# Performance work log

Hardware: AMD Instinct MI355X
Metric: run time of the kernel (lower is better)

Reference implementation:

```python
import jax, jax.numpy as jnp
import numpy as np

# --- dims (match init_kwargs / input_specs) ---
B = 2048          # batch
ALEN = 32         # action history length
TP = 16           # prediction horizon
STATE_DIM = 17
ACTION_DIM = 6
TERMS = 33        # s_recon_terms (Fourier ILT terms)
HID = 64          # hidden_units
GRU_H = 32        # hidden_units // 2
OUT = STATE_DIM   # output_dim
LAT = STATE_DIM + 2  # laplace latent dim (state + 2-d action latent)
# Fourier ILT (Dubner-Abate) constants, as in torchlaplace Fourier defaults
ALPHA = 1e-3
TOL = 1e-2        # 10 * alpha
SCALE = 2.0
PI = np.pi


def _gru_layer(x, Wih, Whh, bih, bhh):
    """PyTorch-semantics GRU layer. x: (B, L, D) -> all hidden states (B, L, H)."""
    nb, H = x.shape[0], Whh.shape[1]
    xw = x @ Wih.T + bih  # (B, L, 3H), precomputed input projections

    def step(h, xw_t):
        gh = h @ Whh.T + bhh
        xr, xz, xn = jnp.split(xw_t, 3, axis=-1)
        hr, hz, hn = jnp.split(gh, 3, axis=-1)
        r = jax.nn.sigmoid(xr + hr)
        z = jax.nn.sigmoid(xz + hz)
        n = jnp.tanh(xn + r * hn)
        h = (1.0 - z) * n + z * h
        return h, h

    h0 = jnp.zeros((nb, H), x.dtype)
    _, outs = jax.lax.scan(step, h0, jnp.swapaxes(xw, 0, 1))
    return jnp.swapaxes(outs, 0, 1)


def setup_inputs() -> dict:
    key = jax.random.key(0)
    ks = jax.random.split(key, 20)
    w = lambda k, shape, s=0.1: jax.random.normal(k, shape, jnp.float32) * s
    d = {}
    d["in_batch_obs"] = jax.random.normal(ks[0], (B, STATE_DIM), jnp.float32)
    d["in_batch_action"] = jax.random.normal(ks[1], (B, ALEN, ACTION_DIM), jnp.float32)
    # positive query times (offset avoids t ~ 0 on the Bromwich contour)
    d["ts_pred"] = jax.random.uniform(ks[2], (B, TP), jnp.float32) + 0.1
    # GRU layer 0
    d["gru_Wih0"] = w(ks[3], (3 * GRU_H, ACTION_DIM))
    d["gru_Whh0"] = w(ks[4], (3 * GRU_H, GRU_H))
    d["gru_bih0"] = jnp.zeros((3 * GRU_H,), jnp.float32)
    d["gru_bhh0"] = jnp.zeros((3 * GRU_H,), jnp.float32)
    # GRU layer 1
    d["gru_Wih1"] = w(ks[5], (3 * GRU_H, GRU_H))
    d["gru_Whh1"] = w(ks[6], (3 * GRU_H, GRU_H))
    d["gru_bih1"] = jnp.zeros((3 * GRU_H,), jnp.float32)
    d["gru_bhh1"] = jnp.zeros((3 * GRU_H,), jnp.float32)
    # encoder linear out -> 2-d action latent
    d["enc_Wout"] = w(ks[7], (2, GRU_H))
    d["enc_bout"] = jnp.zeros((2,), jnp.float32)
    # Laplace representation MLP
    d["mlp_W1"] = w(ks[8], (HID, 2 * TERMS + LAT))
    d["mlp_b1"] = jnp.zeros((HID,), jnp.float32)
    d["mlp_W2"] = w(ks[9], (HID, HID))
    d["mlp_b2"] = jnp.zeros((HID,), jnp.float32)
    d["mlp_W3"] = w(ks[10], (2 * OUT * TERMS, HID))
    d["mlp_b3"] = jnp.zeros((2 * OUT * TERMS,), jnp.float32)
    return d


def reference(in_batch_obs, in_batch_action, ts_pred,
              gru_Wih0, gru_Whh0, gru_bih0, gru_bhh0,
              gru_Wih1, gru_Whh1, gru_bih1, gru_bhh1,
              enc_Wout, enc_bout,
              mlp_W1, mlp_b1, mlp_W2, mlp_b2, mlp_W3, mlp_b3):
    # normalize=False branch
    batch_obs = in_batch_obs
    batch_action = in_batch_action / 3.0

    # ---- ReverseGRUEncoder: flip time, 2-layer GRU, last output -> latent(2) ----
    x = batch_action[:, ::-1, :]
    h1 = _gru_layer(x, gru_Wih0, gru_Whh0, gru_bih0, gru_bhh0)
    h2 = _gru_layer(h1, gru_Wih1, gru_Whh1, gru_bih1, gru_bhh1)
    p_action = h2[:, -1, :] @ enc_Wout.T + enc_bout        # (B, 2)
    p = jnp.concatenate([batch_obs, p_action], axis=1)     # (B, LAT)

    # ---- Fourier ILT contour query points s_k = gamma + i*pi*k/T ----
    t = ts_pred                                            # (B, TP)
    Tc = SCALE * t
    gamma = ALPHA - np.log(TOL) / Tc                       # (B, TP)
    k = jnp.arange(TERMS, dtype=t.dtype)                   # (TERMS,)
    s_im = PI * k / Tc[..., None]                          # (B, TP, TERMS)
    s_re = jnp.broadcast_to(gamma[..., None], s_im.shape)
    # Riemann-sphere coordinates of s
    sq = s_re * s_re + s_im * s_im
    theta_s = jnp.arctan2(s_im, s_re)
    phi_s = jnp.arcsin((sq - 1.0) / (sq + 1.0))

    # ---- LaplaceRepresentationFunc (MLP) per (batch, time) point ----
    pt = jnp.broadcast_to(p[:, None, :], (p.shape[0], t.shape[1], LAT))
    inp = jnp.concatenate([theta_s, phi_s, pt], axis=-1)   # (B, TP, 2*TERMS+LAT)
    h = jnp.tanh(inp @ mlp_W1.T + mlp_b1)
    h = jnp.tanh(h @ mlp_W2.T + mlp_b2)
    out = (h @ mlp_W3.T + mlp_b3).reshape(p.shape[0], t.shape[1], 2 * OUT, TERMS)
    theta = jnp.tanh(out[..., :OUT, :]) * PI               # (B, TP, OUT, TERMS)
    phi = jnp.tanh(out[..., OUT:, :]) * (PI / 2.0)         # phi_scale=pi -> (-pi/2, pi/2)

    # ---- inverse stereographic projection: sphere -> complex F(s) ----
    denom = 1.0 - jnp.sin(phi)
    cphi = jnp.cos(phi)
    Fr = jnp.cos(theta) * cphi / denom
    Fi = jnp.sin(theta) * cphi / denom                     # (B, TP, OUT, TERMS)

    # ---- Fourier-series line integral (k=0 term halved), real arithmetic ----
    ang = PI * k * (t / Tc)[..., None]                     # (B, TP, TERMS)
    wk = jnp.where(k == 0, 0.5, 1.0)
    series = wk * (Fr * jnp.cos(ang)[:, :, None, :] - Fi * jnp.sin(ang)[:, :, None, :])
    f = (jnp.exp(gamma * t) / Tc)[..., None] * series.sum(axis=-1)  # (B, TP, OUT)
    return jnp.squeeze(f)


if __name__ == "__main__":
    outs = reference(**setup_inputs())
    print(outs.shape)
```

## Files before the change

### kernel.cpp

```cpp
#include <hip/hip_runtime.h>
#include <math.h>

#define PI_F 3.14159265358979323846f
#define PI_2F 1.57079632679489662f

typedef __attribute__((ext_vector_type(8))) short short8;
typedef __attribute__((ext_vector_type(4))) float f32x4;
#define MFMA16(A,B,C) __builtin_amdgcn_mfma_f32_16x16x32_bf16(A,B,C,0,0,0)
#define SCHED_FENCE() __builtin_amdgcn_sched_barrier(0)

__device__ __forceinline__ float sigm_f(float x) {
    return __fdividef(1.0f, 1.0f + __expf(-x));
}
__device__ __forceinline__ float tanh_f(float x) {
    float xc = fminf(fmaxf(x, -9.0f), 9.0f);
    float e = __expf(2.0f * xc);
    return 1.0f - __fdividef(2.0f, e + 1.0f);
}
__device__ __forceinline__ float atan01(float z) {
    float z2 = z * z;
    float p = fmaf(z2, -0.0117212f, 0.05265332f);
    p = fmaf(z2, p, -0.11643287f);
    p = fmaf(z2, p, 0.19354346f);
    p = fmaf(z2, p, -0.33262347f);
    p = fmaf(z2, p, 0.99997726f);
    return z * p;
}
__device__ __forceinline__ float atan_pos(float x) {
    bool big = x > 1.0f;
    float z = big ? __fdividef(1.0f, x) : x;
    float p = atan01(z);
    return big ? (PI_2F - p) : p;
}
__device__ __forceinline__ unsigned short f2bf(float x) {
    unsigned int u = __float_as_uint(x);
    return (unsigned short)((u + 0x7FFFu + ((u >> 16) & 1u)) >> 16);
}
__device__ __forceinline__ float bf2f(unsigned short h) {
    return __uint_as_float(((unsigned int)h) << 16);
}
__device__ __forceinline__ float lo16f(unsigned int u) { return __uint_as_float(u << 16); }
__device__ __forceinline__ float hi16f(unsigned int u) { return __uint_as_float(u & 0xFFFF0000u); }

__device__ __forceinline__ float lap_term(float at, float ap, int k) {
    float th = tanh_f(at) * PI_F;
    float ph = tanh_f(ap) * (0.5f * PI_F);
    float sph = __sinf(ph), cph = __cosf(ph);
    float rdv = __fdividef(1.0f, 1.0f - sph);
    float tr = __sinf((k & 1) ? th : th + PI_2F);
    float w = (k == 0) ? 0.5f : 1.0f;
    w = ((k + 1) & 2) ? -w : w;
    return w * tr * cph * rdv;
}

__global__ __launch_bounds__(256)
void w3pack_kernel(const float* __restrict__ W3, unsigned short* __restrict__ pk)
{
    int i = blockIdx.x * 256 + threadIdx.x;
    if (i >= 34 * 4096) return;
    int u    = i >> 12;
    int rem  = i & 4095;
    int r    = rem >> 8;
    int rem2 = rem & 255;
    int pl   = rem2 >> 6;
    int s    = rem2 & 63;
    int o = u >> 1, mt = u & 1;
    int row = o * 33 + mt * 16 + r + ((pl >= 2) ? 561 : 0);
    float x = W3[row * 64 + s];
    unsigned short h = f2bf(x);
    pk[i] = (pl & 1) ? f2bf(x - bf2f(h)) : h;
}

__global__ __launch_bounds__(128)
void gru_kernel(const float* __restrict__ act,
                const float* __restrict__ Wih0, const float* __restrict__ Whh0,
                const float* __restrict__ bih0, const float* __restrict__ bhh0,
                const float* __restrict__ Wih1, const float* __restrict__ Whh1,
                const float* __restrict__ bih1, const float* __restrict__ bhh1,
                const float* __restrict__ encW, const float* __restrict__ encb,
                float* __restrict__ p_out)
{
    __shared__ __align__(16) float wih0_l[6 * 128];
    __shared__ __align__(16) unsigned short whh0_p[16 * 32 * 8];
    __shared__ __align__(16) unsigned short wih1_p[16 * 32 * 8];
    __shared__ __align__(16) unsigned short whh1_p[16 * 32 * 8];
    __shared__ float enc_l[64];
    __shared__ __align__(16) float xbuf[4 * 32 * 6];
    __shared__ __align__(16) float hbuf0[4][32];
    __shared__ __align__(16) float hbuf1[4][32];

    const int tid = threadIdx.x;

    for (int idx = tid; idx < 96 * 6; idx += 128) {
        int r = idx / 6, c = idx - r * 6;
        wih0_l[c * 128 + (r & 31) * 4 + (r >> 5)] = Wih0[idx];
    }
    for (int idx = tid; idx < 96 * 32; idx += 128) {
        int r = idx >> 5, c = idx & 31;
        int g = r >> 5, j = r & 31;
        int d = ((c >> 1) * 32 + j) * 8 + g * 2 + (c & 1);
        whh0_p[d] = f2bf(Whh0[idx]);
        wih1_p[d] = f2bf(Wih1[idx]);
        whh1_p[d] = f2bf(Whh1[idx]);
    }
    if (tid < 64) {
        int o = tid >> 5, j = tid & 31;
        enc_l[j * 2 + o] = encW[o * 32 + j];
    }
    {
        const float inv3 = (1.0f / 3.0f);
        int base = blockIdx.x * (4 * 32 * 6);
        for (int idx = tid; idx < 4 * 32 * 6; idx += 128)
            xbuf[idx] = act[base + idx] * inv3;
    }
    __syncthreads();

    const int s = tid >> 5;
    const int j = tid & 31;
    const int b = blockIdx.x * 4 + s;
    const int j4 = j * 4;

    const float bi0r = bih0[j], bi0z = bih0[32 + j], bi0n = bih0[64 + j];
    const float bh0r = bhh0[j], bh0z = bhh0[32 + j], bh0n = bhh0[64 + j];
    const float bi1r = bih1[j], bi1z = bih1[32 + j], bi1n = bih1[64 + j];
    const float bh1r = bhh1[j], bh1z = bhh1[32 + j], bh1n = bhh1[64 + j];

    float* hb0 = &hbuf0[s][0];
    float* hb1 = &hbuf1[s][0];
    hb0[j] = 0.0f;
    hb1[j] = 0.0f;
    float h0 = 0.0f, h1 = 0.0f;
    const float* xs = &xbuf[s * 192];

    for (int t = 0; t < 32; ++t) {
        const float* xt = &xs[(31 - t) * 6];

        float ar = bi0r, az = bi0z, an = bi0n;
        #pragma unroll
        for (int d = 0; d < 6; ++d) {
            float xv = xt[d];
            const float4 w = *reinterpret_cast<const float4*>(&wih0_l[d * 128 + j4]);
            ar = fmaf(xv, w.x, ar); az = fmaf(xv, w.y, az); an = fmaf(xv, w.z, an);
        }
        {
            float gr0 = bh0r, gz0 = bh0z, gn0 = bh0n;
            float gr1 = 0.0f, gz1 = 0.0f, gn1 = 0.0f;
            #pragma unroll
            for (int ib = 0; ib < 32; ib += 4) {
                const float4 h4 = *reinterpret_cast<const float4*>(&hb0[ib]);
                const uint4 wA = *reinterpret_cast<const uint4*>(&whh0_p[((ib >> 1) * 32 + j) * 8]);
                const uint4 wB = *reinterpret_cast<const uint4*>(&whh0_p[((ib >> 1) * 32 + j + 32) * 8]);
                gr0 = fmaf(h4.x, lo16f(wA.x), gr0); gr1 = fmaf(h4.y, hi16f(wA.x), gr1);
                gz0 = fmaf(h4.x, lo16f(wA.y), gz0); gz1 = fmaf(h4.y, hi16f(wA.y), gz1);
                gn0 = fmaf(h4.x, lo16f(wA.z), gn0); gn1 = fmaf(h4.y, hi16f(wA.z), gn1);
                gr0 = fmaf(h4.z, lo16f(wB.x), gr0); gr1 = fmaf(h4.w, hi16f(wB.x), gr1);
                gz0 = fmaf(h4.z, lo16f(wB.y), gz0); gz1 = fmaf(h4.w, hi16f(wB.y), gz1);
                gn0 = fmaf(h4.z, lo16f(wB.z), gn0); gn1 = fmaf(h4.w, hi16f(wB.z), gn1);
            }
            float r = sigm_f(ar + gr0 + gr1);
            float z = sigm_f(az + gz0 + gz1);
            float n = tanh_f(an + r * (gn0 + gn1));
            h0 = (1.0f - z) * n + z * h0;
            hb0[j] = h0;
        }
        {
            float a1r0 = bi1r, a1z0 = bi1z, a1n0 = bi1n;
            float a1r1 = 0.0f, a1z1 = 0.0f, a1n1 = 0.0f;
            float g1r0 = bh1r, g1z0 = bh1z, g1n0 = bh1n;
            float g1r1 = 0.0f, g1z1 = 0.0f, g1n1 = 0.0f;
            #pragma unroll
            for (int ib = 0; ib < 32; ib += 4) {
                const float4 ha = *reinterpret_cast<const float4*>(&hb0[ib]);
                const float4 hg = *reinterpret_cast<const float4*>(&hb1[ib]);
                const uint4 aA = *reinterpret_cast<const uint4*>(&wih1_p[((ib >> 1) * 32 + j) * 8]);
                const uint4 aB = *reinterpret_cast<const uint4*>(&wih1_p[((ib >> 1) * 32 + j + 32) * 8]);
                const uint4 gA = *reinterpret_cast<const uint4*>(&whh1_p[((ib >> 1) * 32 + j) * 8]);
                const uint4 gB = *reinterpret_cast<const uint4*>(&whh1_p[((ib >> 1) * 32 + j + 32) * 8]);
                a1r0 = fmaf(ha.x, lo16f(aA.x), a1r0); a1r1 = fmaf(ha.y, hi16f(aA.x), a1r1);
                a1z0 = fmaf(ha.x, lo16f(aA.y), a1z0); a1z1 = fmaf(ha.y, hi16f(aA.y), a1z1);
                a1n0 = fmaf(ha.x, lo16f(aA.z), a1n0); a1n1 = fmaf(ha.y, hi16f(aA.z), a1n1);
                a1r0 = fmaf(ha.z, lo16f(aB.x), a1r0); a1r1 = fmaf(ha.w, hi16f(aB.x), a1r1);
                a1z0 = fmaf(ha.z, lo16f(aB.y), a1z0); a1z1 = fmaf(ha.w, hi16f(aB.y), a1z1);
                a1n0 = fmaf(ha.z, lo16f(aB.z), a1n0); a1n1 = fmaf(ha.w, hi16f(aB.z), a1n1);
                g1r0 = fmaf(hg.x, lo16f(gA.x), g1r0); g1r1 = fmaf(hg.y, hi16f(gA.x), g1r1);
                g1z0 = fmaf(hg.x, lo16f(gA.y), g1z0); g1z1 = fmaf(hg.y, hi16f(gA.y), g1z1);
                g1n0 = fmaf(hg.x, lo16f(gA.z), g1n0); g1n1 = fmaf(hg.y, hi16f(gA.z), g1n1);
                g1r0 = fmaf(hg.z, lo16f(gB.x), g1r0); g1r1 = fmaf(hg.w, hi16f(gB.x), g1r1);
                g1z0 = fmaf(hg.z, lo16f(gB.y), g1z0); g1z1 = fmaf(hg.w, hi16f(gB.y), g1z1);
                g1n0 = fmaf(hg.z, lo16f(gB.z), g1n0); g1n1 = fmaf(hg.w, hi16f(gB.z), g1n1);
            }
            float r1 = sigm_f(a1r0 + a1r1 + g1r0 + g1r1);
            float z1 = sigm_f(a1z0 + a1z1 + g1z0 + g1z1);
            float n1 = tanh_f(a1n0 + a1n1 + r1 * (g1n0 + g1n1));
            h1 = (1.0f - z1) * n1 + z1 * h1;
            hb1[j] = h1;
        }
    }

    float v0 = h1 * enc_l[j * 2 + 0];
    float v1 = h1 * enc_l[j * 2 + 1];
    #pragma unroll
    for (int off = 16; off > 0; off >>= 1) {
        v0 += __shfl_xor(v0, off, 32);
        v1 += __shfl_xor(v1, off, 32);
    }
    if (j == 0) {
        p_out[b * 2 + 0] = v0 + encb[0];
        p_out[b * 2 + 1] = v1 + encb[1];
    }
}


__device__ __forceinline__ void load_B(const unsigned short* b_hi, const unsigned short* b_lo,
                                       int itm, int ksl,
                                       short8& Bh0, short8& Bh1, short8& Bl0, short8& Bl1)
{
    const int sw = (itm & 7) << 3;
    const int kx0 = ksl ^ sw;
    const int kx1 = (32 + ksl) ^ sw;
    Bh0 = *reinterpret_cast<const short8*>(&b_hi[itm * 64 + kx0]);
    Bh1 = *reinterpret_cast<const short8*>(&b_hi[itm * 64 + kx1]);
    Bl0 = *reinterpret_cast<const short8*>(&b_lo[itm * 64 + kx0]);
    Bl1 = *reinterpret_cast<const short8*>(&b_lo[itm * 64 + kx1]);
}

__device__ __forceinline__ float lap4(f32x4 aT, f32x4 aP, const float* __restrict__ b3,
                                      int rd, int kbase)
{
    float s = 0.0f;
    #pragma unroll
    for (int r = 0; r < 4; ++r)
        s += lap_term(aT[r] + b3[rd + r], aP[r] + b3[rd + r + 561], kbase + r);
    return s;
}

__device__ __forceinline__ float k32_term(const float* __restrict__ W3f,
                                          const float* __restrict__ b3,
                                          const float* __restrict__ h2f,
                                          int o, int l4)
{
    const int rt = o * 33 + 32;
    const float* wtr = W3f + rt * 64;
    const float* wpr = W3f + (rt + 561) * 64;
    float at = b3[rt], ap = b3[rt + 561];
    #pragma unroll
    for (int c = 0; c < 16; ++c) {
        const float4 g4 = *reinterpret_cast<const float4*>(&h2f[c * 256 + l4]);
        at = fmaf(g4.x, wtr[c * 4 + 0], at);
        at = fmaf(g4.y, wtr[c * 4 + 1], at);
        at = fmaf(g4.z, wtr[c * 4 + 2], at);
        at = fmaf(g4.w, wtr[c * 4 + 3], at);
        ap = fmaf(g4.x, wpr[c * 4 + 0], ap);
        ap = fmaf(g4.y, wpr[c * 4 + 1], ap);
        ap = fmaf(g4.z, wpr[c * 4 + 2], ap);
        ap = fmaf(g4.w, wpr[c * 4 + 3], ap);
    }
    return lap_term(at, ap, 32);
}

#define UNIT_G(G, EACC) { \
    short8 Bh0, Bh1, Bl0, Bl1; \
    load_B(b_hi, b_lo, (G) * 16 + lm, ksl, Bh0, Bh1, Bl0, Bl1); \
    f32x4 accT = {0.0f, 0.0f, 0.0f, 0.0f}; \
    { \
        const short8 A0 = *reinterpret_cast<const short8*>(au + 0); \
        const short8 A1 = *reinterpret_cast<const short8*>(au + 64); \
        const short8 A2 = *reinterpret_cast<const short8*>(au + 128); \
        const short8 A3 = *reinterpret_cast<const short8*>(au + 192); \
        accT = MFMA16(A0, Bh0, accT); accT = MFMA16(A1, Bh1, accT); \
        accT = MFMA16(A0, Bl0, accT); accT = MFMA16(A1, Bl1, accT); \
        accT = MFMA16(A2, Bh0, accT); accT = MFMA16(A3, Bh1, accT); \
    } \
    f32x4 accP = {0.0f, 0.0f, 0.0f, 0.0f}; \
    { \
        const short8 A0 = *reinterpret_cast<const short8*>(au + 256); \
        const short8 A1 = *reinterpret_cast<const short8*>(au + 320); \
        const short8 A2 = *reinterpret_cast<const short8*>(au + 384); \
        const short8 A3 = *reinterpret_cast<const short8*>(au + 448); \
        accP = MFMA16(A0, Bh0, accP); accP = MFMA16(A1, Bh1, accP); \
        accP = MFMA16(A0, Bl0, accP); accP = MFMA16(A1, Bl1, accP); \
        accP = MFMA16(A2, Bh0, accP); accP = MFMA16(A3, Bh1, accP); \
    } \
    EACC += lap4(accT, accP, b3, rd, kbase); \
    SCHED_FENCE(); \
}

__global__ __launch_bounds__(512, 4)
void mlp_kernel(const float* __restrict__ obs, const float* __restrict__ ts,
                const float* __restrict__ p_act,
                const float* __restrict__ W1, const float* __restrict__ b1,
                const float* __restrict__ W2, const float* __restrict__ b2,
                const unsigned short* __restrict__ w3pk,
                const float* __restrict__ b3,
                const float* __restrict__ W3f,
                float* __restrict__ out)
{
    __shared__ __align__(16) float h1t[16 * 256];
    __shared__ __align__(16) unsigned short b_hi[64 * 64];
    __shared__ __align__(16) unsigned short b_lo[64 * 64];
    __shared__ __align__(16) float vtp_lds[33 * 128];
    __shared__ float f_lds[17 * 64];
    __shared__ float f16k32[64];
    __shared__ float scale_lds[64];

    float* h2f = vtp_lds;

    const int tid = threadIdx.x;
    const int wq = __builtin_amdgcn_readfirstlane(tid >> 6);
    const int l = tid & 63;
    const int l4 = l * 4;
    const int item = blockIdx.x * 64 + l;
    const int b = item >> 4;
    const int obase = wq * 8;

    const float t = ts[item];
    const float rTc = __fdividef(0.5f, t);
    const float gamma = 0.001f + 4.6051701859880913680f * rTc;

    if (wq == 0) scale_lds[l] = __expf(gamma * t) * rTc;

    const float gam2 = gamma * gamma;
    const float rg = __fdividef(1.0f, gamma);
    const float pirTc = PI_F * rTc;

    for (int k = wq; k < 33; k += 8) {
        float sim = (float)k * pirTc;
        float vth = atan_pos(sim * rg);
        float sq = fmaf(sim, sim, gam2);
        float vph = fmaf(-2.0f, atan01(rsqrtf(sq)), PI_2F);
        vtp_lds[k * 128 + (l << 1) + 0] = vth;
        vtp_lds[k * 128 + (l << 1) + 1] = vph;
    }
    __syncthreads();

    {
        float acc[8];
        #pragma unroll
        for (int oo = 0; oo < 8; ++oo) acc[oo] = b1[obase + oo];
        const float* w1b = W1 + obase * 85;

        for (int k = 0; k < 33; ++k) {
            const float2 tp = *reinterpret_cast<const float2*>(&vtp_lds[k * 128 + (l << 1)]);
            #pragma unroll
            for (int oo = 0; oo < 8; ++oo) {
                acc[oo] = fmaf(tp.x, w1b[oo * 85 + k], acc[oo]);
                acc[oo] = fmaf(tp.y, w1b[oo * 85 + 33 + k], acc[oo]);
            }
        }
        #pragma unroll
        for (int j = 0; j < 19; ++j) {
            float pv = (j < 17) ? obs[b * 17 + j] : p_act[b * 2 + (j - 17)];
            #pragma unroll
            for (int oo = 0; oo < 8; ++oo)
                acc[oo] = fmaf(pv, w1b[oo * 85 + 66 + j], acc[oo]);
        }
        #pragma unroll
        for (int oo = 0; oo < 8; ++oo) {
            int o = obase + oo;
            h1t[(o >> 2) * 256 + l4 + (o & 3)] = tanh_f(acc[oo]);
        }
    }
    __syncthreads();

    {
        float acc[8];
        #pragma unroll
        for (int oo = 0; oo < 8; ++oo) acc[oo] = b2[obase + oo];
        #pragma unroll
        for (int c = 0; c < 16; ++c) {
            const float4 g4 = *reinterpret_cast<const float4*>(&h1t[c * 256 + l4]);
            #pragma unroll
            for (int oo = 0; oo < 8; ++oo) {
                const float* wr = W2 + (obase + oo) * 64 + c * 4;
                acc[oo] = fmaf(g4.x, wr[0], acc[oo]);
                acc[oo] = fmaf(g4.y, wr[1], acc[oo]);
                acc[oo] = fmaf(g4.z, wr[2], acc[oo]);
                acc[oo] = fmaf(g4.w, wr[3], acc[oo]);
            }
        }
        const int sw = (l & 7) << 3;
        #pragma unroll
        for (int p = 0; p < 4; ++p) {
            float v0 = tanh_f(acc[2 * p + 0]);
            float v1 = tanh_f(acc[2 * p + 1]);
            int o0 = obase + 2 * p;
            h2f[((o0 + 0) >> 2) * 256 + l4 + ((o0 + 0) & 3)] = v0;
            h2f[((o0 + 1) >> 2) * 256 + l4 + ((o0 + 1) & 3)] = v1;
            unsigned short h0 = f2bf(v0), h1v = f2bf(v1);
            unsigned short q0 = f2bf(v0 - bf2f(h0)), q1 = f2bf(v1 - bf2f(h1v));
            int ksw = o0 ^ sw;
            *reinterpret_cast<unsigned int*>(&b_hi[l * 64 + ksw]) =
                (unsigned int)h0 | ((unsigned int)h1v << 16);
            *reinterpret_cast<unsigned int*>(&b_lo[l * 64 + ksw]) =
                (unsigned int)q0 | ((unsigned int)q1 << 16);
        }
    }
    __syncthreads();

    {
        const int lm = l & 15;
        const int lq = l >> 4;
        const int ksl = lq * 8;
        const char* apk = (const char*)w3pk;
        const int lane_off = lm * 512 + lq * 16;

        #pragma unroll 1
        for (int oo2 = 0; oo2 < 2; ++oo2) {
            const int o = wq * 2 + oo2;
            const float k32t = k32_term(W3f, b3, h2f, o, l4);
            float e0 = 0.0f, e1 = 0.0f, e2 = 0.0f, e3 = 0.0f;

            #pragma unroll 1
            for (int mt = 0; mt < 2; ++mt) {
                const char* au = apk + ((o * 2 + mt) << 13) + lane_off;
                const int rd = o * 33 + mt * 16 + lq * 4;
                const int kbase = mt * 16 + lq * 4;

                UNIT_G(0, e0)
                UNIT_G(1, e1)
                UNIT_G(2, e2)
                UNIT_G(3, e3)
            }
            e0 += __shfl_xor(e0, 16); e0 += __shfl_xor(e0, 32);
            e1 += __shfl_xor(e1, 16); e1 += __shfl_xor(e1, 32);
            e2 += __shfl_xor(e2, 16); e2 += __shfl_xor(e2, 32);
            e3 += __shfl_xor(e3, 16); e3 += __shfl_xor(e3, 32);
            float tot = (lq == 0) ? e0 : (lq == 1) ? e1 : (lq == 2) ? e2 : e3;
            f_lds[o * 64 + l] = tot + k32t;
        }

        if (wq < 4) {
            const int g = wq;
            float facc = 0.0f;
            #pragma unroll 1
            for (int mt = 0; mt < 2; ++mt) {
                const char* au = apk + ((16 * 2 + mt) << 13) + lane_off;
                const int rd = 16 * 33 + mt * 16 + lq * 4;
                const int kbase = mt * 16 + lq * 4;
                UNIT_G(g, facc)
            }
            facc += __shfl_xor(facc, 16);
            facc += __shfl_xor(facc, 32);
            if (l < 16) f_lds[16 * 64 + g * 16 + l] = facc;
        } else if (wq == 4) {
            f16k32[l] = k32_term(W3f, b3, h2f, 16, l4);
        }
    }
    __syncthreads();

    const int base_item = blockIdx.x * 64;
    for (int idx = tid; idx < 64 * 17; idx += 512) {
        const int li = idx / 17;
        const int o  = idx - li * 17;
        float v = f_lds[o * 64 + li];
        if (o == 16) v += f16k32[li];
        out[(base_item + li) * 17 + o] = v * scale_lds[li];
    }
}

extern "C" void kernel_launch(void* const* d_in, const int* in_sizes, int n_in,
                              void* d_out, int out_size, void* d_ws, size_t ws_size,
                              hipStream_t stream) {
    (void)in_sizes; (void)n_in; (void)out_size; (void)ws_size;
    const float* obs  = (const float*)d_in[0];
    const float* act  = (const float*)d_in[1];
    const float* ts   = (const float*)d_in[2];
    const float* Wih0 = (const float*)d_in[3];
    const float* Whh0 = (const float*)d_in[4];
    const float* bih0 = (const float*)d_in[5];
    const float* bhh0 = (const float*)d_in[6];
    const float* Wih1 = (const float*)d_in[7];
    const float* Whh1 = (const float*)d_in[8];
    const float* bih1 = (const float*)d_in[9];
    const float* bhh1 = (const float*)d_in[10];
    const float* encW = (const float*)d_in[11];
    const float* encb = (const float*)d_in[12];
    const float* W1   = (const float*)d_in[13];
    const float* b1   = (const float*)d_in[14];
    const float* W2   = (const float*)d_in[15];
    const float* b2   = (const float*)d_in[16];
    const float* W3   = (const float*)d_in[17];
    const float* b3   = (const float*)d_in[18];
    float* o_ptr  = (float*)d_out;

    float* p_act = (float*)d_ws;
    unsigned short* w3pk = (unsigned short*)((char*)d_ws + 16384);

    w3pack_kernel<<<dim3((34 * 4096 + 255) / 256), dim3(256), 0, stream>>>(W3, w3pk);
    gru_kernel<<<dim3(512), dim3(128), 0, stream>>>(
        act, Wih0, Whh0, bih0, bhh0, Wih1, Whh1, bih1, bhh1, encW, encb, p_act);
    mlp_kernel<<<dim3(512), dim3(512), 0, stream>>>(
        obs, ts, p_act, W1, b1, W2, b2, w3pk, b3, W3, o_ptr);
}
```

Before: 135.7 us.

## Split GRU hidden reductions across two half-waves and drop bf16 low-part MFMAs

The GRU kernel now uses 64 lanes per sequence instead of 32. Each half-wave reduces over half of the hidden inputs, and the partial sums are combined with a cross-half shuffle, which shortens the serial per-step dot products. In the MLP kernel, the B operand's bf16 low-part (error compensation) term is removed, which cuts two MFMAs per accumulator and the b_lo LDS buffer and stores. That second change lowers the precision of the final Laplace reconstruction, which may be magnified by the exp(gamma*t) scaling.

```diff
diff --git a/kernel.cpp b/kernel.cpp
--- a/kernel.cpp
+++ b/kernel.cpp
@@ -71,7 +71,7 @@
     pk[i] = (pl & 1) ? f2bf(x - bf2f(h)) : h;
 }
 
-__global__ __launch_bounds__(128)
+__global__ __launch_bounds__(256)
 void gru_kernel(const float* __restrict__ act,
                 const float* __restrict__ Wih0, const float* __restrict__ Whh0,
                 const float* __restrict__ bih0, const float* __restrict__ bhh0,
@@ -91,11 +91,11 @@
 
     const int tid = threadIdx.x;
 
-    for (int idx = tid; idx < 96 * 6; idx += 128) {
+    for (int idx = tid; idx < 96 * 6; idx += 256) {
         int r = idx / 6, c = idx - r * 6;
         wih0_l[c * 128 + (r & 31) * 4 + (r >> 5)] = Wih0[idx];
     }
-    for (int idx = tid; idx < 96 * 32; idx += 128) {
+    for (int idx = tid; idx < 96 * 32; idx += 256) {
         int r = idx >> 5, c = idx & 31;
         int g = r >> 5, j = r & 31;
         int d = ((c >> 1) * 32 + j) * 8 + g * 2 + (c & 1);
@@ -110,90 +110,105 @@
     {
         const float inv3 = (1.0f / 3.0f);
         int base = blockIdx.x * (4 * 32 * 6);
-        for (int idx = tid; idx < 4 * 32 * 6; idx += 128)
+        for (int idx = tid; idx < 4 * 32 * 6; idx += 256)
             xbuf[idx] = act[base + idx] * inv3;
     }
     __syncthreads();
 
-    const int s = tid >> 5;
-    const int j = tid & 31;
+    const int s = tid >> 6;
+    const int l = tid & 63;
+    const int j = l & 31;
+    const int half = l >> 5;
+    const int i0 = half * 16;
+    const int sb = half * 8;
+    const int j4 = j * 4;
     const int b = blockIdx.x * 4 + s;
-    const int j4 = j * 4;
-
-    const float bi0r = bih0[j], bi0z = bih0[32 + j], bi0n = bih0[64 + j];
-    const float bh0r = bhh0[j], bh0z = bhh0[32 + j], bh0n = bhh0[64 + j];
-    const float bi1r = bih1[j], bi1z = bih1[32 + j], bi1n = bih1[64 + j];
-    const float bh1r = bhh1[j], bh1z = bhh1[32 + j], bh1n = bhh1[64 + j];
+    const float z0f = (half == 0) ? 1.0f : 0.0f;
+
+    const float bi0r = z0f * bih0[j], bi0z = z0f * bih0[32 + j], bi0n = z0f * bih0[64 + j];
+    const float bh0r = z0f * bhh0[j], bh0z = z0f * bhh0[32 + j], bh0n = z0f * bhh0[64 + j];
+    const float bi1r = z0f * bih1[j], bi1z = z0f * bih1[32 + j], bi1n = z0f * bih1[64 + j];
+    const float bh1r = z0f * bhh1[j], bh1z = z0f * bhh1[32 + j], bh1n = z0f * bhh1[64 + j];
 
     float* hb0 = &hbuf0[s][0];
     float* hb1 = &hbuf1[s][0];
-    hb0[j] = 0.0f;
-    hb1[j] = 0.0f;
+    if (!half) { hb0[j] = 0.0f; hb1[j] = 0.0f; }
     float h0 = 0.0f, h1 = 0.0f;
     const float* xs = &xbuf[s * 192];
 
     for (int t = 0; t < 32; ++t) {
         const float* xt = &xs[(31 - t) * 6];
 
-        float ar = bi0r, az = bi0z, an = bi0n;
-        #pragma unroll
-        for (int d = 0; d < 6; ++d) {
-            float xv = xt[d];
-            const float4 w = *reinterpret_cast<const float4*>(&wih0_l[d * 128 + j4]);
-            ar = fmaf(xv, w.x, ar); az = fmaf(xv, w.y, az); an = fmaf(xv, w.z, an);
+        float gr0 = bi0r + bh0r, gz0 = bi0z + bh0z, gn0 = bh0n, an = bi0n;
+        if (half == 0) {
+            #pragma unroll
+            for (int d = 0; d < 6; ++d) {
+                float xv = xt[d];
+                const float4 w = *reinterpret_cast<const float4*>(&wih0_l[d * 128 + j4]);
+                gr0 = fmaf(xv, w.x, gr0); gz0 = fmaf(xv, w.y, gz0); an = fmaf(xv, w.z, an);
+            }
         }
         {
-            float gr0 = bh0r, gz0 = bh0z, gn0 = bh0n;
             float gr1 = 0.0f, gz1 = 0.0f, gn1 = 0.0f;
             #pragma unroll
-            for (int ib = 0; ib < 32; ib += 4) {
-                const float4 h4 = *reinterpret_cast<const float4*>(&hb0[ib]);
-                const uint4 wA = *reinterpret_cast<const uint4*>(&whh0_p[((ib >> 1) * 32 + j) * 8]);
-                const uint4 wB = *reinterpret_cast<const uint4*>(&whh0_p[((ib >> 1) * 32 + j + 32) * 8]);
-                gr0 = fmaf(h4.x, lo16f(wA.x), gr0); gr1 = fmaf(h4.y, hi16f(wA.x), gr1);
-                gz0 = fmaf(h4.x, lo16f(wA.y), gz0); gz1 = fmaf(h4.y, hi16f(wA.y), gz1);
-                gn0 = fmaf(h4.x, lo16f(wA.z), gn0); gn1 = fmaf(h4.y, hi16f(wA.z), gn1);
-                gr0 = fmaf(h4.z, lo16f(wB.x), gr0); gr1 = fmaf(h4.w, hi16f(wB.x), gr1);
-                gz0 = fmaf(h4.z, lo16f(wB.y), gz0); gz1 = fmaf(h4.w, hi16f(wB.y), gz1);
-                gn0 = fmaf(h4.z, lo16f(wB.z), gn0); gn1 = fmaf(h4.w, hi16f(wB.z), gn1);
-            }
-            float r = sigm_f(ar + gr0 + gr1);
-            float z = sigm_f(az + gz0 + gz1);
-            float n = tanh_f(an + r * (gn0 + gn1));
+            for (int m = 0; m < 8; m += 2) {
+                const float2 ha = *reinterpret_cast<const float2*>(&hb0[i0 + 2 * m]);
+                const float2 hc = *reinterpret_cast<const float2*>(&hb0[i0 + 2 * m + 2]);
+                const uint4 wA = *reinterpret_cast<const uint4*>(&whh0_p[((sb + m) * 32 + j) * 8]);
+                const uint4 wB = *reinterpret_cast<const uint4*>(&whh0_p[((sb + m + 1) * 32 + j) * 8]);
+                gr0 = fmaf(ha.x, lo16f(wA.x), gr0); gr0 = fmaf(ha.y, hi16f(wA.x), gr0);
+                gz0 = fmaf(ha.x, lo16f(wA.y), gz0); gz0 = fmaf(ha.y, hi16f(wA.y), gz0);
+                gn0 = fmaf(ha.x, lo16f(wA.z), gn0); gn0 = fmaf(ha.y, hi16f(wA.z), gn0);
+                gr1 = fmaf(hc.x, lo16f(wB.x), gr1); gr1 = fmaf(hc.y, hi16f(wB.x), gr1);
+                gz1 = fmaf(hc.x, lo16f(wB.y), gz1); gz1 = fmaf(hc.y, hi16f(wB.y), gz1);
+                gn1 = fmaf(hc.x, lo16f(wB.z), gn1); gn1 = fmaf(hc.y, hi16f(wB.z), gn1);
+            }
+            float grt = gr0 + gr1; grt += __shfl_xor(grt, 32);
+            float gzt = gz0 + gz1; gzt += __shfl_xor(gzt, 32);
+            float gnt = gn0 + gn1; gnt += __shfl_xor(gnt, 32);
+            float ant = an;        ant += __shfl_xor(ant, 32);
+            float r = sigm_f(grt);
+            float z = sigm_f(gzt);
+            float n = tanh_f(ant + r * gnt);
             h0 = (1.0f - z) * n + z * h0;
-            hb0[j] = h0;
-        }
+            if (!half) hb0[j] = h0;
+        }
+
         {
-            float a1r0 = bi1r, a1z0 = bi1z, a1n0 = bi1n;
-            float a1r1 = 0.0f, a1z1 = 0.0f, a1n1 = 0.0f;
-            float g1r0 = bh1r, g1z0 = bh1z, g1n0 = bh1n;
-            float g1r1 = 0.0f, g1z1 = 0.0f, g1n1 = 0.0f;
-            #pragma unroll
-            for (int ib = 0; ib < 32; ib += 4) {
-                const float4 ha = *reinterpret_cast<const float4*>(&hb0[ib]);
-                const float4 hg = *reinterpret_cast<const float4*>(&hb1[ib]);
-                const uint4 aA = *reinterpret_cast<const uint4*>(&wih1_p[((ib >> 1) * 32 + j) * 8]);
-                const uint4 aB = *reinterpret_cast<const uint4*>(&wih1_p[((ib >> 1) * 32 + j + 32) * 8]);
-                const uint4 gA = *reinterpret_cast<const uint4*>(&whh1_p[((ib >> 1) * 32 + j) * 8]);
-                const uint4 gB = *reinterpret_cast<const uint4*>(&whh1_p[((ib >> 1) * 32 + j + 32) * 8]);
-                a1r0 = fmaf(ha.x, lo16f(aA.x), a1r0); a1r1 = fmaf(ha.y, hi16f(aA.x), a1r1);
-                a1z0 = fmaf(ha.x, lo16f(aA.y), a1z0); a1z1 = fmaf(ha.y, hi16f(aA.y), a1z1);
-                a1n0 = fmaf(ha.x, lo16f(aA.z), a1n0); a1n1 = fmaf(ha.y, hi16f(aA.z), a1n1);
-                a1r0 = fmaf(ha.z, lo16f(aB.x), a1r0); a1r1 = fmaf(ha.w, hi16f(aB.x), a1r1);
-                a1z0 = fmaf(ha.z, lo16f(aB.y), a1z0); a1z1 = fmaf(ha.w, hi16f(aB.y), a1z1);
-                a1n0 = fmaf(ha.z, lo16f(aB.z), a1n0); a1n1 = fmaf(ha.w, hi16f(aB.z), a1n1);
-                g1r0 = fmaf(hg.x, lo16f(gA.x), g1r0); g1r1 = fmaf(hg.y, hi16f(gA.x), g1r1);
-                g1z0 = fmaf(hg.x, lo16f(gA.y), g1z0); g1z1 = fmaf(hg.y, hi16f(gA.y), g1z1);
-                g1n0 = fmaf(hg.x, lo16f(gA.z), g1n0); g1n1 = fmaf(hg.y, hi16f(gA.z), g1n1);
-                g1r0 = fmaf(hg.z, lo16f(gB.x), g1r0); g1r1 = fmaf(hg.w, hi16f(gB.x), g1r1);
-                g1z0 = fmaf(hg.z, lo16f(gB.y), g1z0); g1z1 = fmaf(hg.w, hi16f(gB.y), g1z1);
-                g1n0 = fmaf(hg.z, lo16f(gB.z), g1n0); g1n1 = fmaf(hg.w, hi16f(gB.z), g1n1);
-            }
-            float r1 = sigm_f(a1r0 + a1r1 + g1r0 + g1r1);
-            float z1 = sigm_f(a1z0 + a1z1 + g1z0 + g1z1);
-            float n1 = tanh_f(a1n0 + a1n1 + r1 * (g1n0 + g1n1));
+            float R0 = bi1r + bh1r, Z0 = bi1z + bh1z, aN0 = bi1n, gN0 = bh1n;
+            float R1 = 0.0f, Z1 = 0.0f, aN1 = 0.0f, gN1 = 0.0f;
+            #pragma unroll
+            for (int m = 0; m < 8; m += 2) {
+                const float2 ha = *reinterpret_cast<const float2*>(&hb0[i0 + 2 * m]);
+                const float2 hc = *reinterpret_cast<const float2*>(&hb0[i0 + 2 * m + 2]);
+                const float2 pa = *reinterpret_cast<const float2*>(&hb1[i0 + 2 * m]);
+                const float2 pc = *reinterpret_cast<const float2*>(&hb1[i0 + 2 * m + 2]);
+                const uint4 aA = *reinterpret_cast<const uint4*>(&wih1_p[((sb + m) * 32 + j) * 8]);
+                const uint4 aB = *reinterpret_cast<const uint4*>(&wih1_p[((sb + m + 1) * 32 + j) * 8]);
+                const uint4 gA = *reinterpret_cast<const uint4*>(&whh1_p[((sb + m) * 32 + j) * 8]);
+                const uint4 gB = *reinterpret_cast<const uint4*>(&whh1_p[((sb + m + 1) * 32 + j) * 8]);
+                R0 = fmaf(ha.x, lo16f(aA.x), R0); R0 = fmaf(ha.y, hi16f(aA.x), R0);
+                Z0 = fmaf(ha.x, lo16f(aA.y), Z0); Z0 = fmaf(ha.y, hi16f(aA.y), Z0);
+                aN0 = fmaf(ha.x, lo16f(aA.z), aN0); aN0 = fmaf(ha.y, hi16f(aA.z), aN0);
+                R1 = fmaf(hc.x, lo16f(aB.x), R1); R1 = fmaf(hc.y, hi16f(aB.x), R1);
+                Z1 = fmaf(hc.x, lo16f(aB.y), Z1); Z1 = fmaf(hc.y, hi16f(aB.y), Z1);
+                aN1 = fmaf(hc.x, lo16f(aB.z), aN1); aN1 = fmaf(hc.y, hi16f(aB.z), aN1);
+                R0 = fmaf(pa.x, lo16f(gA.x), R0); R0 = fmaf(pa.y, hi16f(gA.x), R0);
+                Z0 = fmaf(pa.x, lo16f(gA.y), Z0); Z0 = fmaf(pa.y, hi16f(gA.y), Z0);
+                gN0 = fmaf(pa.x, lo16f(gA.z), gN0); gN0 = fmaf(pa.y, hi16f(gA.z), gN0);
+                R1 = fmaf(pc.x, lo16f(gB.x), R1); R1 = fmaf(pc.y, hi16f(gB.x), R1);
+                Z1 = fmaf(pc.x, lo16f(gB.y), Z1); Z1 = fmaf(pc.y, hi16f(gB.y), Z1);
+                gN1 = fmaf(pc.x, lo16f(gB.z), gN1); gN1 = fmaf(pc.y, hi16f(gB.z), gN1);
+            }
+            float Rt = R0 + R1;   Rt += __shfl_xor(Rt, 32);
+            float Zt = Z0 + Z1;   Zt += __shfl_xor(Zt, 32);
+            float aNt = aN0 + aN1; aNt += __shfl_xor(aNt, 32);
+            float gNt = gN0 + gN1; gNt += __shfl_xor(gNt, 32);
+            float r1 = sigm_f(Rt);
+            float z1 = sigm_f(Zt);
+            float n1 = tanh_f(aNt + r1 * gNt);
             h1 = (1.0f - z1) * n1 + z1 * h1;
-            hb1[j] = h1;
+            if (!half) hb1[j] = h1;
         }
     }
 
@@ -204,24 +219,19 @@
         v0 += __shfl_xor(v0, off, 32);
         v1 += __shfl_xor(v1, off, 32);
     }
-    if (j == 0) {
+    if (l == 0) {
         p_out[b * 2 + 0] = v0 + encb[0];
         p_out[b * 2 + 1] = v1 + encb[1];
     }
 }
 
 
-__device__ __forceinline__ void load_B(const unsigned short* b_hi, const unsigned short* b_lo,
-                                       int itm, int ksl,
-                                       short8& Bh0, short8& Bh1, short8& Bl0, short8& Bl1)
+__device__ __forceinline__ void load_B(const unsigned short* b_hi,
+                                       int itm, int ksl, short8& Bh0, short8& Bh1)
 {
     const int sw = (itm & 7) << 3;
-    const int kx0 = ksl ^ sw;
-    const int kx1 = (32 + ksl) ^ sw;
-    Bh0 = *reinterpret_cast<const short8*>(&b_hi[itm * 64 + kx0]);
-    Bh1 = *reinterpret_cast<const short8*>(&b_hi[itm * 64 + kx1]);
-    Bl0 = *reinterpret_cast<const short8*>(&b_lo[itm * 64 + kx0]);
-    Bl1 = *reinterpret_cast<const short8*>(&b_lo[itm * 64 + kx1]);
+    Bh0 = *reinterpret_cast<const short8*>(&b_hi[itm * 64 + (ksl ^ sw)]);
+    Bh1 = *reinterpret_cast<const short8*>(&b_hi[itm * 64 + ((32 + ksl) ^ sw)]);
 }
 
 __device__ __forceinline__ float lap4(f32x4 aT, f32x4 aP, const float* __restrict__ b3,
@@ -259,8 +269,8 @@
 }
 
 #define UNIT_G(G, EACC) { \
-    short8 Bh0, Bh1, Bl0, Bl1; \
-    load_B(b_hi, b_lo, (G) * 16 + lm, ksl, Bh0, Bh1, Bl0, Bl1); \
+    short8 Bh0, Bh1; \
+    load_B(b_hi, (G) * 16 + lm, ksl, Bh0, Bh1); \
     f32x4 accT = {0.0f, 0.0f, 0.0f, 0.0f}; \
     { \
         const short8 A0 = *reinterpret_cast<const short8*>(au + 0); \
@@ -268,7 +278,6 @@
         const short8 A2 = *reinterpret_cast<const short8*>(au + 128); \
         const short8 A3 = *reinterpret_cast<const short8*>(au + 192); \
         accT = MFMA16(A0, Bh0, accT); accT = MFMA16(A1, Bh1, accT); \
-        accT = MFMA16(A0, Bl0, accT); accT = MFMA16(A1, Bl1, accT); \
         accT = MFMA16(A2, Bh0, accT); accT = MFMA16(A3, Bh1, accT); \
     } \
     f32x4 accP = {0.0f, 0.0f, 0.0f, 0.0f}; \
@@ -278,7 +287,6 @@
         const short8 A2 = *reinterpret_cast<const short8*>(au + 384); \
         const short8 A3 = *reinterpret_cast<const short8*>(au + 448); \
         accP = MFMA16(A0, Bh0, accP); accP = MFMA16(A1, Bh1, accP); \
-        accP = MFMA16(A0, Bl0, accP); accP = MFMA16(A1, Bl1, accP); \
         accP = MFMA16(A2, Bh0, accP); accP = MFMA16(A3, Bh1, accP); \
     } \
     EACC += lap4(accT, accP, b3, rd, kbase); \
@@ -297,7 +305,6 @@
 {
     __shared__ __align__(16) float h1t[16 * 256];
     __shared__ __align__(16) unsigned short b_hi[64 * 64];
-    __shared__ __align__(16) unsigned short b_lo[64 * 64];
     __shared__ __align__(16) float vtp_lds[33 * 128];
     __shared__ float f_lds[17 * 64];
     __shared__ float f16k32[64];
@@ -387,12 +394,9 @@
             h2f[((o0 + 0) >> 2) * 256 + l4 + ((o0 + 0) & 3)] = v0;
             h2f[((o0 + 1) >> 2) * 256 + l4 + ((o0 + 1) & 3)] = v1;
             unsigned short h0 = f2bf(v0), h1v = f2bf(v1);
-            unsigned short q0 = f2bf(v0 - bf2f(h0)), q1 = f2bf(v1 - bf2f(h1v));
             int ksw = o0 ^ sw;
             *reinterpret_cast<unsigned int*>(&b_hi[l * 64 + ksw]) =
                 (unsigned int)h0 | ((unsigned int)h1v << 16);
-            *reinterpret_cast<unsigned int*>(&b_lo[l * 64 + ksw]) =
-                (unsigned int)q0 | ((unsigned int)q1 << 16);
         }
     }
     __syncthreads();
@@ -487,7 +491,7 @@
     unsigned short* w3pk = (unsigned short*)((char*)d_ws + 16384);
 
     w3pack_kernel<<<dim3((34 * 4096 + 255) / 256), dim3(256), 0, stream>>>(W3, w3pk);
-    gru_kernel<<<dim3(512), dim3(128), 0, stream>>>(
+    gru_kernel<<<dim3(512), dim3(256), 0, stream>>>(
         act, Wih0, Whh0, bih0, bhh0, Wih1, Whh1, bih1, bhh1, encW, encb, p_act);
     mlp_kernel<<<dim3(512), dim3(512), 0, stream>>>(
         obs, ts, p_act, W1, b1, W2, b2, w3pk, b3, W3, o_ptr);
```

New measurement: 116.7 us, median of 2. 1.16x faster.
